# Kernel optimization log

Measured on AMD Instinct MI355X. Metric: run time of the kernel, lower is better.

Reference implementation:

```python
import jax, jax.numpy as jnp
import numpy as np

B, A, M, C = 8, 100000, 32, 80
IMG = 512.0


def setup_inputs():
    key = jax.random.key(0)
    k1, k2, k3, k4, k5, k6, k7, k8 = jax.random.split(key, 8)
    classifications = jax.random.uniform(k1, (B, A, C), jnp.float32)  # sigmoid-like probs
    regressions = jax.random.normal(k2, (B, A, 4), jnp.float32)
    # anchors: valid boxes (x1<x2, y1<y2) from centers + sizes
    ctr = jax.random.uniform(k3, (A, 2), jnp.float32, 0.0, IMG)
    wh = jax.random.uniform(k4, (A, 2), jnp.float32, 16.0, 256.0)
    anchors = jnp.concatenate([ctr - wh / 2, ctr + wh / 2], axis=-1)[None]  # [1,A,4]
    # annotations: [B,M,6] = x1,y1,x2,y2,class,aux_label (all valid, no -1 padding)
    gctr = jax.random.uniform(k5, (B, M, 2), jnp.float32, 32.0, IMG - 32.0)
    gwh = jax.random.uniform(k6, (B, M, 2), jnp.float32, 8.0, 128.0)
    boxes = jnp.concatenate([gctr - gwh / 2, gctr + gwh / 2], axis=-1)
    cls_ids = jax.random.randint(k7, (B, M, 1), 0, C).astype(jnp.float32)
    aux = jax.random.randint(k8, (B, M, 1), 0, 2).astype(jnp.float32)
    annotations = jnp.concatenate([boxes, cls_ids, aux], axis=-1)
    return {"classifications": classifications, "regressions": regressions,
            "anchors": anchors, "annotations": annotations}


def calc_iou(a, b):
    # a: [A,4] anchors, b: [M,4] gt boxes -> [A,M]
    area_a = ((a[:, 2] - a[:, 0]) * (a[:, 3] - a[:, 1]))[:, None]
    area_b = (b[:, 2] - b[:, 0]) * (b[:, 3] - b[:, 1])
    iw = jnp.minimum(a[:, 2:3], b[None, :, 2]) - jnp.maximum(a[:, 0:1], b[None, :, 0])
    ih = jnp.minimum(a[:, 3:4], b[None, :, 3]) - jnp.maximum(a[:, 1:2], b[None, :, 1])
    inter = jnp.clip(iw, 0.0) * jnp.clip(ih, 0.0)
    ua = jnp.clip(area_a + area_b[None, :] - inter, 1e-8)
    return inter / ua


def reference(classifications, regressions, anchors, annotations):
    alpha, gamma = 0.25, 2.0
    anchor = anchors[0]  # [A,4]
    aw = anchor[:, 2] - anchor[:, 0]
    ah = anchor[:, 3] - anchor[:, 1]
    acx = anchor[:, 0] + 0.5 * aw
    acy = anchor[:, 1] + 0.5 * ah
    std = jnp.array([0.1, 0.1, 0.2, 0.2], jnp.float32)

    def per_image(cls, reg, ann):
        valid = ann[:, 4] != -1.0  # padding mask (replaces dynamic filter)
        iou = calc_iou(anchor, ann[:, :4])  # [A,M]
        iou = jnp.where(valid[None, :], iou, -1.0)
        iou_max = iou.max(axis=1)
        iou_argmax = iou.argmax(axis=1)
        assigned = ann[iou_argmax]  # [A,6]
        cls = jnp.clip(cls, 1e-4, 1.0 - 1e-4)
        pos = iou_max >= 0.5
        num_pos = pos.sum().astype(jnp.float32)
        one_hot = jax.nn.one_hot(assigned[:, 4].astype(jnp.int32), cls.shape[1], dtype=cls.dtype)
        targets = jnp.where(pos[:, None], one_hot,
                            jnp.where((iou_max < 0.4)[:, None], 0.0, -1.0))
        alpha_factor = jnp.where(targets == 1.0, alpha, 1.0 - alpha)
        focal_w = alpha_factor * jnp.where(targets == 1.0, 1.0 - cls, cls) ** gamma
        bce = -(targets * jnp.log(cls) + (1.0 - targets) * jnp.log(1.0 - cls))
        cls_loss = jnp.where(targets != -1.0, focal_w * bce, 0.0)
        cls_loss = cls_loss.sum() / jnp.maximum(num_pos, 1.0)
        gw = assigned[:, 2] - assigned[:, 0]
        gh = assigned[:, 3] - assigned[:, 1]
        gcx = assigned[:, 0] + 0.5 * gw
        gcy = assigned[:, 1] + 0.5 * gh
        gw = jnp.clip(gw, 1.0)
        gh = jnp.clip(gh, 1.0)
        t = jnp.stack([(gcx - acx) / aw, (gcy - acy) / ah,
                       jnp.log(gw / aw), jnp.log(gh / ah)], axis=1) / std
        diff = jnp.abs(t - reg)
        rl = jnp.where(diff <= 1.0 / 9.0, 0.5 * 9.0 * diff ** 2, diff - 0.5 / 9.0)
        rl = jnp.where(pos[:, None], rl, 0.0)
        reg_loss = jnp.where(num_pos > 0,
                             rl.sum() / (4.0 * jnp.maximum(num_pos, 1.0)), 0.0)
        return cls_loss, reg_loss

    cl, rl = jax.vmap(per_image)(classifications, regressions, annotations)
    return cl.mean(keepdims=True), rl.mean(keepdims=True)
```

## Files before the change

### kernel.cpp

```cpp
#include <hip/hip_runtime.h>
#include <math.h>

#define B_IMG   8
#define A_ANCH  100000
#define M_ANN   32
#define C_CLS   80
#define TILE    256
#define NTHREADS 256
#define NWAVES  (NTHREADS/64)
#define V_PER_ANCH (C_CLS/4)

__global__ void focal_init(float* __restrict__ ws) {
    int i = threadIdx.x;
    if (i < 3 * B_IMG) ws[i] = 0.0f;
}

__device__ __forceinline__ float focal4(float4 p4, int code, int c0) {
    const float m = (code != -1) ? 1.0f : 0.0f;
    float acc = 0.0f;
    const float pv[4] = {p4.x, p4.y, p4.z, p4.w};
    #pragma unroll
    for (int j = 0; j < 4; ++j) {
        const float p = fminf(fmaxf(pv[j], 1e-4f), 1.0f - 1e-4f);
        const bool t1 = (code == c0 + j);
        const float q = t1 ? (1.0f - p) : p;
        const float w = t1 ? 0.25f : 0.75f;
        acc = fmaf(m * w * q * q, -__logf(1.0f - q), acc);
    }
    return acc;
}

__global__ __launch_bounds__(NTHREADS)
void focal_main(const float* __restrict__ cls,
                const float* __restrict__ regr,
                const float* __restrict__ anchors,
                const float* __restrict__ ann,
                float* __restrict__ ws)
{
    __shared__ float s_ann[M_ANN][6];
    __shared__ float s_area[M_ANN];
    __shared__ int   s_code[TILE];
    __shared__ float s_red[3][NWAVES];

    const int b  = blockIdx.y;
    const int a0 = blockIdx.x * TILE;
    const int t  = threadIdx.x;

    if (t < M_ANN * 6) ((float*)s_ann)[t] = ann[(size_t)b * M_ANN * 6 + t];
    __syncthreads();
    if (t < M_ANN)
        s_area[t] = (s_ann[t][2] - s_ann[t][0]) * (s_ann[t][3] - s_ann[t][1]);
    __syncthreads();

    float reg_acc = 0.0f;
    float pos_cnt = 0.0f;

    const int a = a0 + t;
    if (a < A_ANCH) {
        const float4 ab = ((const float4*)anchors)[a];
        const float aw = ab.z - ab.x;
        const float ah = ab.w - ab.y;
        const float acx = ab.x + 0.5f * aw;
        const float acy = ab.y + 0.5f * ah;
        const float area_a = aw * ah;

        float best = -2.0f;
        int   bm   = 0;
        #pragma unroll 8
        for (int m = 0; m < M_ANN; ++m) {
            float iou;
            if (s_ann[m][4] == -1.0f) {
                iou = -1.0f;
            } else {
                float iw = fminf(ab.z, s_ann[m][2]) - fmaxf(ab.x, s_ann[m][0]);
                float ih = fminf(ab.w, s_ann[m][3]) - fmaxf(ab.y, s_ann[m][1]);
                float inter = fmaxf(iw, 0.0f) * fmaxf(ih, 0.0f);
                float ua = fmaxf(area_a + s_area[m] - inter, 1e-8f);
                iou = inter / ua;
            }
            if (iou > best) { best = iou; bm = m; }
        }

        const bool pos = (best >= 0.5f);
        int code;
        if (pos)                 code = (int)s_ann[bm][4];
        else if (best < 0.4f)    code = -2;
        else                     code = -1;
        s_code[t] = code;

        if (pos) {
            pos_cnt = 1.0f;
            const float gx1 = s_ann[bm][0], gy1 = s_ann[bm][1];
            const float gx2 = s_ann[bm][2], gy2 = s_ann[bm][3];
            float gw = gx2 - gx1, gh = gy2 - gy1;
            const float gcx = gx1 + 0.5f * gw;
            const float gcy = gy1 + 0.5f * gh;
            gw = fmaxf(gw, 1.0f); gh = fmaxf(gh, 1.0f);
            const float t0 = (gcx - acx) / aw * 10.0f;
            const float t1v = (gcy - acy) / ah * 10.0f;
            const float t2 = logf(gw / aw) * 5.0f;
            const float t3 = logf(gh / ah) * 5.0f;

            const float4 rg = ((const float4*)regr)[(size_t)b * A_ANCH + a];
            const float d0 = fabsf(t0  - rg.x);
            const float d1 = fabsf(t1v - rg.y);
            const float d2 = fabsf(t2  - rg.z);
            const float d3 = fabsf(t3  - rg.w);
            const float th = 1.0f / 9.0f;
            const float c_ = 0.5f / 9.0f;
            reg_acc += (d0 <= th) ? 4.5f * d0 * d0 : d0 - c_;
            reg_acc += (d1 <= th) ? 4.5f * d1 * d1 : d1 - c_;
            reg_acc += (d2 <= th) ? 4.5f * d2 * d2 : d2 - c_;
            reg_acc += (d3 <= th) ? 4.5f * d3 * d3 : d3 - c_;
        }
    } else {
        s_code[t] = -1;
    }
    __syncthreads();

    float cls_acc = 0.0f;
    const int n_anch = min(TILE, A_ANCH - a0);
    const float4* cbase = (const float4*)(cls + ((size_t)b * A_ANCH + a0) * C_CLS);

    if (n_anch == TILE) {
        #pragma unroll
        for (int kk = 0; kk < 4; ++kk) {
            float4 r[5];
            int    vv[5];
            #pragma unroll
            for (int u = 0; u < 5; ++u) {
                vv[u] = t + (kk * 5 + u) * NTHREADS;
                r[u]  = cbase[vv[u]];
            }
            #pragma unroll
            for (int u = 0; u < 5; ++u) {
                const int v  = vv[u];
                const int al = v / V_PER_ANCH;
                const int c0 = (v - al * V_PER_ANCH) * 4;
                cls_acc += focal4(r[u], s_code[al], c0);
            }
        }
    } else {
        const int nv = n_anch * V_PER_ANCH;
        for (int v = t; v < nv; v += NTHREADS) {
            const int al = v / V_PER_ANCH;
            const int c0 = (v - al * V_PER_ANCH) * 4;
            cls_acc += focal4(cbase[v], s_code[al], c0);
        }
    }

    #pragma unroll
    for (int off = 32; off > 0; off >>= 1) {
        cls_acc += __shfl_down(cls_acc, off, 64);
        reg_acc += __shfl_down(reg_acc, off, 64);
        pos_cnt += __shfl_down(pos_cnt, off, 64);
    }
    const int wave = t >> 6, lane = t & 63;
    if (lane == 0) {
        s_red[0][wave] = cls_acc;
        s_red[1][wave] = reg_acc;
        s_red[2][wave] = pos_cnt;
    }
    __syncthreads();
    if (t == 0) {
        float c = 0.f, r = 0.f, p = 0.f;
        #pragma unroll
        for (int w = 0; w < NWAVES; ++w) { c += s_red[0][w]; r += s_red[1][w]; p += s_red[2][w]; }
        atomicAdd(&ws[b * 3 + 0], c);
        atomicAdd(&ws[b * 3 + 1], r);
        atomicAdd(&ws[b * 3 + 2], p);
    }
}

__global__ void focal_final(const float* __restrict__ ws, float* __restrict__ out) {
    if (threadIdx.x == 0) {
        float cl = 0.f, rl = 0.f;
        for (int b = 0; b < B_IMG; ++b) {
            const float np  = ws[b * 3 + 2];
            const float mnp = fmaxf(np, 1.0f);
            cl += ws[b * 3 + 0] / mnp;
            rl += (np > 0.0f) ? ws[b * 3 + 1] / (4.0f * mnp) : 0.0f;
        }
        out[0] = cl / (float)B_IMG;
        out[1] = rl / (float)B_IMG;
    }
}

extern "C" void kernel_launch(void* const* d_in, const int* in_sizes, int n_in,
                              void* d_out, int out_size, void* d_ws, size_t ws_size,
                              hipStream_t stream) {
    const float* cls     = (const float*)d_in[0];
    const float* regr    = (const float*)d_in[1];
    const float* anchors = (const float*)d_in[2];
    const float* ann     = (const float*)d_in[3];
    float* out = (float*)d_out;
    float* ws  = (float*)d_ws;

    focal_init<<<1, 64, 0, stream>>>(ws);

    dim3 grid((A_ANCH + TILE - 1) / TILE, B_IMG);
    focal_main<<<grid, NTHREADS, 0, stream>>>(cls, regr, anchors, ann, ws);

    focal_final<<<1, 64, 0, stream>>>(ws, out);
}
```

Measured before the change: 406.4 us.

## Stage classification tiles into LDS via async global_load_lds double buffering

Replaces the direct per-thread float4 global loads of classification probabilities with asynchronous global-to-LDS copies into a two-slot staging buffer. The first chunk is issued before the IoU matching loop so its latency can hide behind the anchor-assignment work. Each later chunk is prefetched while the previous one is consumed. The cost is 32 KB of extra LDS per block, which can lower occupancy, plus an extra barrier per chunk; the overlap relies on __syncthreads also waiting for the outstanding loads.

```diff
diff --git a/kernel.cpp b/kernel.cpp
--- a/kernel.cpp
+++ b/kernel.cpp
@@ -9,6 +9,10 @@
 #define NTHREADS 256
 #define NWAVES  (NTHREADS/64)
 #define V_PER_ANCH (C_CLS/4)
+
+#define CHUNK_F4   1024
+#define NITER      5
+#define F4_PER_THR 4
 
 __global__ void focal_init(float* __restrict__ ws) {
     int i = threadIdx.x;
@@ -37,20 +41,41 @@
                 const float* __restrict__ ann,
                 float* __restrict__ ws)
 {
-    __shared__ float s_ann[M_ANN][6];
-    __shared__ float s_area[M_ANN];
-    __shared__ int   s_code[TILE];
-    __shared__ float s_red[3][NWAVES];
-
-    const int b  = blockIdx.y;
-    const int a0 = blockIdx.x * TILE;
-    const int t  = threadIdx.x;
+    __shared__ float  s_ann[M_ANN][6];
+    __shared__ float  s_area[M_ANN];
+    __shared__ int    s_code[TILE];
+    __shared__ float  s_red[3][NWAVES];
+    __shared__ float4 s_stage[2][CHUNK_F4];
+
+    const int b    = blockIdx.y;
+    const int a0   = blockIdx.x * TILE;
+    const int t    = threadIdx.x;
+    const int wave = t >> 6;
+    const int lane = t & 63;
+
+    const int n_anch = min(TILE, A_ANCH - a0);
+    const bool full  = (n_anch == TILE);
+    const float4* cbase = (const float4*)(cls + ((size_t)b * A_ANCH + a0) * C_CLS);
 
     if (t < M_ANN * 6) ((float*)s_ann)[t] = ann[(size_t)b * M_ANN * 6 + t];
     __syncthreads();
     if (t < M_ANN)
         s_area[t] = (s_ann[t][2] - s_ann[t][0]) * (s_ann[t][3] - s_ann[t][1]);
-    __syncthreads();
+
+    auto issue_chunk = [&](int c, int p) {
+        const char* gch = (const char*)cbase + (size_t)c * (CHUNK_F4 * 16);
+        #pragma unroll
+        for (int u = 0; u < F4_PER_THR; ++u) {
+            const int off = __builtin_amdgcn_readfirstlane((wave * F4_PER_THR + u) * 1024);
+            const char* src = gch + off + lane * 16;
+            char* dst = (char*)&s_stage[p][0] + off;
+            __builtin_amdgcn_global_load_lds(
+                (const __attribute__((address_space(1))) void*)src,
+                (__attribute__((address_space(3))) void*)dst,
+                16, 0, 0);
+        }
+    };
+    if (full) issue_chunk(0, 0);
 
     float reg_acc = 0.0f;
     float pos_cnt = 0.0f;
@@ -119,26 +144,21 @@
     __syncthreads();
 
     float cls_acc = 0.0f;
-    const int n_anch = min(TILE, A_ANCH - a0);
-    const float4* cbase = (const float4*)(cls + ((size_t)b * A_ANCH + a0) * C_CLS);
-
-    if (n_anch == TILE) {
+    if (full) {
         #pragma unroll
-        for (int kk = 0; kk < 4; ++kk) {
-            float4 r[5];
-            int    vv[5];
+        for (int it = 0; it < NITER; ++it) {
+            const int p = it & 1;
+            if (it + 1 < NITER) issue_chunk(it + 1, p ^ 1);
             #pragma unroll
-            for (int u = 0; u < 5; ++u) {
-                vv[u] = t + (kk * 5 + u) * NTHREADS;
-                r[u]  = cbase[vv[u]];
-            }
-            #pragma unroll
-            for (int u = 0; u < 5; ++u) {
-                const int v  = vv[u];
+            for (int u = 0; u < F4_PER_THR; ++u) {
+                const int idx = t + u * NTHREADS;
+                const float4 p4 = s_stage[p][idx];
+                const int v  = it * CHUNK_F4 + idx;
                 const int al = v / V_PER_ANCH;
                 const int c0 = (v - al * V_PER_ANCH) * 4;
-                cls_acc += focal4(r[u], s_code[al], c0);
+                cls_acc += focal4(p4, s_code[al], c0);
             }
+            if (it + 1 < NITER) __syncthreads();
         }
     } else {
         const int nv = n_anch * V_PER_ANCH;
@@ -155,7 +175,6 @@
         reg_acc += __shfl_down(reg_acc, off, 64);
         pos_cnt += __shfl_down(pos_cnt, off, 64);
     }
-    const int wave = t >> 6, lane = t & 63;
     if (lane == 0) {
         s_red[0][wave] = cls_acc;
         s_red[1][wave] = reg_acc;
```

New measurement: 398.5 us. Within noise of the previous version (-1.9%).
